# Optimization experiments

Measured on AMD Instinct MI355X. Metric: run time of the kernel, lower is better.

## Reference

```python
import jax, jax.numpy as jnp
import numpy as np
import math

IN_FEATURES = 4096
OUT_FEATURES = 4096
TOKENS = 8192


def hadamard(x):
    """Orthonormal fast Walsh-Hadamard transform along last dim (power of two)."""
    n = x.shape[-1]
    orig_shape = x.shape
    y = x.reshape(-1, n)
    h = 1
    while h < n:  # log2(n) butterfly steps (static loop, n known at trace time)
        y = y.reshape(-1, n // (2 * h), 2 * h)
        left = y[..., :h]
        right = y[..., h:2 * h]
        y = jnp.concatenate([left + right, left - right], axis=-1)
        y = y.reshape(-1, n)
        h *= 2
    return (y / math.sqrt(n)).reshape(orig_shape)


def setup_inputs() -> dict:
    key = jax.random.key(0)
    k1, k2, k3, k4 = jax.random.split(key, 4)
    x = jax.random.normal(k1, (TOKENS, IN_FEATURES), dtype=jnp.float32)
    # int8-valued quantized weights, stored as int32 for portability
    Q_tilde = jax.random.randint(k2, (OUT_FEATURES, IN_FEATURES), -127, 128, dtype=jnp.int32)
    # per-row scales, positive, realistic magnitude (~max_abs/127)
    s_tilde = jax.random.uniform(k3, (OUT_FEATURES, 1), dtype=jnp.float32, minval=0.001, maxval=0.02)
    bias = jax.random.normal(k4, (OUT_FEATURES,), dtype=jnp.float32)
    return {"x": x, "Q_tilde": Q_tilde, "s_tilde": s_tilde, "bias": bias}


def reference(x, Q_tilde, s_tilde, bias):
    # y = hadamard(x) @ (Q * s)^T + bias
    xh = hadamard(x)                                      # [T, in]
    W = Q_tilde.astype(jnp.float32) * s_tilde             # [out, in] dequantized
    y = xh @ W.T + bias                                   # [T, out]
    return y
```

## Files before the change

### kernel.cpp

```cpp
#include <hip/hip_runtime.h>
#include <hip/hip_bf16.h>

typedef int   i32x4 __attribute__((ext_vector_type(4)));
typedef unsigned int   u32;
typedef unsigned short u16;
typedef signed char    i8;

#define TOKENS 8192
#define NDIM   4096
#define KDIM   4096
#define BK     64
#define NKT    (KDIM / BK)

__global__ __launch_bounds__(64)
void fwht_rows_q8(const float* __restrict__ x, i8* __restrict__ xq,
                  float* __restrict__ xscale) {
  const int row = blockIdx.x;
  const int l   = threadIdx.x;

  const float4* xv = reinterpret_cast<const float4*>(x + (size_t)row * KDIM) + l * 16;
  float v[64];
#pragma unroll
  for (int j = 0; j < 16; ++j) {
    float4 f = xv[j];
    v[4*j+0] = f.x; v[4*j+1] = f.y; v[4*j+2] = f.z; v[4*j+3] = f.w;
  }

#pragma unroll
  for (int h = 1; h < 64; h <<= 1) {
#pragma unroll
    for (int j = 0; j < 64; ++j) {
      if ((j & h) == 0) {
        float a = v[j], b = v[j + h];
        v[j] = a + b; v[j + h] = a - b;
      }
    }
  }

#pragma unroll
  for (int m = 1; m < 64; m <<= 1) {
    const bool up = (l & m) != 0;
#pragma unroll
    for (int j = 0; j < 64; ++j) {
      float p = __shfl_xor(v[j], m, 64);
      v[j] = up ? (p - v[j]) : (v[j] + p);
    }
  }

  float mxu = 0.f;
#pragma unroll
  for (int j = 0; j < 64; ++j) mxu = fmaxf(mxu, fabsf(v[j]));
#pragma unroll
  for (int m = 1; m < 64; m <<= 1) mxu = fmaxf(mxu, __shfl_xor(mxu, m, 64));
  mxu = fmaxf(mxu, 1e-30f);
  const float inv = 127.0f / mxu;

  i8* orow = xq + (size_t)row * KDIM + l * 64;
#pragma unroll
  for (int g = 0; g < 4; ++g) {
    u32 w[4];
#pragma unroll
    for (int q4 = 0; q4 < 4; ++q4) {
      int b0 = __float2int_rn(v[g*16+q4*4+0] * inv);
      int b1 = __float2int_rn(v[g*16+q4*4+1] * inv);
      int b2 = __float2int_rn(v[g*16+q4*4+2] * inv);
      int b3 = __float2int_rn(v[g*16+q4*4+3] * inv);
      b0 = min(127, max(-127, b0)); b1 = min(127, max(-127, b1));
      b2 = min(127, max(-127, b2)); b3 = min(127, max(-127, b3));
      w[q4] = (u32)(b0 & 0xff) | ((u32)(b1 & 0xff) << 8) |
              ((u32)(b2 & 0xff) << 16) | ((u32)(b3 & 0xff) << 24);
    }
    uint4 pk; pk.x = w[0]; pk.y = w[1]; pk.z = w[2]; pk.w = w[3];
    *reinterpret_cast<uint4*>(orow + g * 16) = pk;
  }
  if (l == 0) xscale[row] = mxu * (0.015625f / 127.0f);
}

__device__ __forceinline__ u32 pack4(int4 q) {
  return (u32)(q.x & 0xff) | ((u32)(q.y & 0xff) << 8) |
         ((u32)(q.z & 0xff) << 16) | ((u32)(q.w & 0xff) << 24);
}
__global__ __launch_bounds__(256)
void qpack(const int* __restrict__ Q, i8* __restrict__ W8) {
  const size_t idx = ((size_t)blockIdx.x * 256 + threadIdx.x) * 16;
  int4 a = *reinterpret_cast<const int4*>(Q + idx);
  int4 b = *reinterpret_cast<const int4*>(Q + idx + 4);
  int4 c = *reinterpret_cast<const int4*>(Q + idx + 8);
  int4 d = *reinterpret_cast<const int4*>(Q + idx + 12);
  uint4 pk; pk.x = pack4(a); pk.y = pack4(b); pk.z = pack4(c); pk.w = pack4(d);
  *reinterpret_cast<uint4*>(W8 + idx) = pk;
}

__global__ __launch_bounds__(512, 2)
void gemm256_i8(const i8* __restrict__ A, const i8* __restrict__ B,
                const float* __restrict__ xscale, const float* __restrict__ s,
                const float* __restrict__ bias, float* __restrict__ C) {
  __shared__ __align__(16) i8 lds[4 * 32768];

  const int th   = threadIdx.x;
  const int wave = th >> 6;
  const int lane = th & 63;

  const int b0 = blockIdx.x;
  const int xc = b0 & 7;
  const int i  = b0 >> 3;
  const int mt = i >> 1;
  const int nt = xc * 2 + (i & 1);

  const int srow = th >> 2;
  const int scol = ((th & 3) * 16) ^ (((th >> 5) & 1) << 5);
  const i8* gA0 = A + (size_t)(mt * 256 + srow) * KDIM + scol;
  const i8* gA1 = gA0 + (size_t)128 * KDIM;
  const i8* gB0 = B + (size_t)(nt * 256 + srow) * KDIM + scol;
  const i8* gB1 = gB0 + (size_t)128 * KDIM;

  const int ldsA0 = wave * 1024;
  const int ldsA1 = 8192 + wave * 1024;
  const int ldsB0 = 16384 + wave * 1024;
  const int ldsB1 = 24576 + wave * 1024;

#define STAGE_A(tt, ss) do {                                                    \
    __builtin_amdgcn_global_load_lds(                                           \
      (const __attribute__((address_space(1))) void*)(gA0 + (size_t)(tt) * BK), \
      (__attribute__((address_space(3))) void*)(lds + (ss) * 32768 + ldsA0), 16, 0, 0); \
    __builtin_amdgcn_global_load_lds(                                           \
      (const __attribute__((address_space(1))) void*)(gA1 + (size_t)(tt) * BK), \
      (__attribute__((address_space(3))) void*)(lds + (ss) * 32768 + ldsA1), 16, 0, 0); \
  } while (0)
#define STAGE_B(tt, ss) do {                                                    \
    __builtin_amdgcn_global_load_lds(                                           \
      (const __attribute__((address_space(1))) void*)(gB0 + (size_t)(tt) * BK), \
      (__attribute__((address_space(3))) void*)(lds + (ss) * 32768 + ldsB0), 16, 0, 0); \
    __builtin_amdgcn_global_load_lds(                                           \
      (const __attribute__((address_space(1))) void*)(gB1 + (size_t)(tt) * BK), \
      (__attribute__((address_space(3))) void*)(lds + (ss) * 32768 + ldsB1), 16, 0, 0); \
  } while (0)

  const int wm = wave >> 2;
  const int wn = wave & 3;
  const int laneRow = lane & 15;
  const int kByte   = (lane >> 4) << 4;
  const int swz     = ((lane >> 3) & 1) << 5;
  const int aOff = (((wm * 128 + laneRow) * 64 + kByte) ^ swz);
  const int bOff = (((wn * 64 + laneRow) * 64 + kByte) ^ swz) + 16384;

  i32x4 acc[8][4];
#pragma unroll
  for (int mi = 0; mi < 8; ++mi)
#pragma unroll
    for (int ni = 0; ni < 4; ++ni)
      acc[mi][ni] = i32x4{0, 0, 0, 0};

  STAGE_A(0, 0); STAGE_B(0, 0);
  STAGE_A(1, 1); STAGE_B(1, 1);
  asm volatile("s_waitcnt vmcnt(4)" ::: "memory");
  __builtin_amdgcn_sched_barrier(0);
  __builtin_amdgcn_s_barrier();

  for (int t = 0; t < NKT; ++t) {
    const char* base = (const char*)lds + (t & 3) * 32768;
    i32x4 bfr[4], af[4];

#pragma unroll
    for (int ni = 0; ni < 4; ++ni)
      bfr[ni] = *(const i32x4*)(base + bOff + ni * 1024);
#pragma unroll
    for (int mi = 0; mi < 4; ++mi)
      af[mi] = *(const i32x4*)(base + aOff + mi * 1024);
    if (t + 2 < NKT) { STAGE_A(t + 2, (t + 2) & 3); STAGE_B(t + 2, (t + 2) & 3); }
    __builtin_amdgcn_s_barrier();
    asm volatile("s_waitcnt lgkmcnt(0)" ::: "memory");
    __builtin_amdgcn_sched_barrier(0);
    __builtin_amdgcn_s_setprio(1);
#pragma unroll
    for (int mi = 0; mi < 4; ++mi)
#pragma unroll
      for (int ni = 0; ni < 4; ++ni)
        acc[mi][ni] = __builtin_amdgcn_mfma_i32_16x16x64_i8(af[mi], bfr[ni], acc[mi][ni], 0, 0, 0);
    __builtin_amdgcn_s_setprio(0);
    __builtin_amdgcn_s_barrier();

#pragma unroll
    for (int mi = 0; mi < 4; ++mi)
      af[mi] = *(const i32x4*)(base + aOff + 4096 + mi * 1024);
    if (t + 2 < NKT) asm volatile("s_waitcnt vmcnt(4)" ::: "memory");
    else             asm volatile("s_waitcnt vmcnt(0)" ::: "memory");
    __builtin_amdgcn_sched_barrier(0);
    __builtin_amdgcn_s_barrier();
    asm volatile("s_waitcnt lgkmcnt(0)" ::: "memory");
    __builtin_amdgcn_sched_barrier(0);
    __builtin_amdgcn_s_setprio(1);
#pragma unroll
    for (int mi = 0; mi < 4; ++mi)
#pragma unroll
      for (int ni = 0; ni < 4; ++ni)
        acc[mi + 4][ni] = __builtin_amdgcn_mfma_i32_16x16x64_i8(af[mi], bfr[ni], acc[mi + 4][ni], 0, 0, 0);
    __builtin_amdgcn_s_setprio(0);
    __builtin_amdgcn_s_barrier();
  }
#undef STAGE_A
#undef STAGE_B

  const int col0 = nt * 256 + wn * 64 + (lane & 15);
  const int row0 = mt * 256 + wm * 128 + ((lane >> 4) << 2);
  float xs[4][8];
#pragma unroll
  for (int mi = 0; mi < 8; ++mi)
#pragma unroll
    for (int r = 0; r < 4; ++r)
      xs[r][mi] = xscale[row0 + mi * 16 + r];
#pragma unroll
  for (int ni = 0; ni < 4; ++ni) {
    const float sc = s[col0 + ni * 16];
    const float bv = bias[col0 + ni * 16];
#pragma unroll
    for (int mi = 0; mi < 8; ++mi) {
      float* cp = C + (size_t)(row0 + mi * 16) * NDIM + col0 + ni * 16;
#pragma unroll
      for (int r = 0; r < 4; ++r)
        cp[(size_t)r * NDIM] = (float)acc[mi][ni][r] * (xs[r][mi] * sc) + bv;
    }
  }
}

extern "C" void kernel_launch(void* const* d_in, const int* in_sizes, int n_in,
                              void* d_out, int out_size, void* d_ws, size_t ws_size,
                              hipStream_t stream) {
  (void)in_sizes; (void)n_in; (void)out_size; (void)ws_size;
  const float* x    = (const float*)d_in[0];
  const int*   Q    = (const int*)d_in[1];
  const float* s    = (const float*)d_in[2];
  const float* bias = (const float*)d_in[3];
  float* out = (float*)d_out;

  i8*    xq     = (i8*)d_ws;
  i8*    W8     = xq + (size_t)TOKENS * KDIM;
  float* xscale = (float*)(W8 + (size_t)NDIM * KDIM);

  fwht_rows_q8<<<dim3(TOKENS), dim3(64), 0, stream>>>(x, xq, xscale);
  qpack<<<dim3((NDIM * KDIM) / (256 * 16)), dim3(256), 0, stream>>>(Q, W8);
  gemm256_i8<<<dim3((TOKENS / 256) * (NDIM / 256)), dim3(512), 0, stream>>>(
      xq, W8, xscale, s, bias, out);
}
```

Measured before the change: 210.7 us.

## Fuse FWHT and weight-pack kernels; restructure GEMM to BK=128 double-buffered pipeline

Merges the row Hadamard/quantize kernel and the int32-to-int8 weight pack kernel into one launch, using block-index ranges and four rows per 256-thread block. The GEMM now stages 128-wide K tiles into two 64 KB LDS buffers. It software-pipelines the fragment reads by preloading the next tile's A/B registers and interleaving partial lgkmcnt waits with MFMA groups, so each iteration needs one barrier instead of four. The aim is to cut launch overhead and sync stalls. The cost is a shallower two-stage prefetch and more live registers.

```diff
diff --git a/kernel.cpp b/kernel.cpp
--- a/kernel.cpp
+++ b/kernel.cpp
@@ -9,14 +9,29 @@
 #define TOKENS 8192
 #define NDIM   4096
 #define KDIM   4096
-#define BK     64
-#define NKT    (KDIM / BK)
-
-__global__ __launch_bounds__(64)
-void fwht_rows_q8(const float* __restrict__ x, i8* __restrict__ xq,
-                  float* __restrict__ xscale) {
-  const int row = blockIdx.x;
-  const int l   = threadIdx.x;
+#define NKT2   32
+
+__device__ __forceinline__ u32 pack4(int4 q) {
+  return (u32)(q.x & 0xff) | ((u32)(q.y & 0xff) << 8) |
+         ((u32)(q.z & 0xff) << 16) | ((u32)(q.w & 0xff) << 24);
+}
+
+__global__ __launch_bounds__(256)
+void fused_aux(const float* __restrict__ x, i8* __restrict__ xq,
+               float* __restrict__ xscale,
+               const int* __restrict__ Q, i8* __restrict__ W8) {
+  if (blockIdx.x >= 2048) {
+    const size_t idx = (((size_t)(blockIdx.x - 2048)) * 256 + threadIdx.x) * 16;
+    int4 a = *reinterpret_cast<const int4*>(Q + idx);
+    int4 b = *reinterpret_cast<const int4*>(Q + idx + 4);
+    int4 c = *reinterpret_cast<const int4*>(Q + idx + 8);
+    int4 d = *reinterpret_cast<const int4*>(Q + idx + 12);
+    uint4 pk; pk.x = pack4(a); pk.y = pack4(b); pk.z = pack4(c); pk.w = pack4(d);
+    *reinterpret_cast<uint4*>(W8 + idx) = pk;
+    return;
+  }
+  const int row = blockIdx.x * 4 + (threadIdx.x >> 6);
+  const int l   = threadIdx.x & 63;
 
   const float4* xv = reinterpret_cast<const float4*>(x + (size_t)row * KDIM) + l * 16;
   float v[64];
@@ -76,26 +91,11 @@
   if (l == 0) xscale[row] = mxu * (0.015625f / 127.0f);
 }
 
-__device__ __forceinline__ u32 pack4(int4 q) {
-  return (u32)(q.x & 0xff) | ((u32)(q.y & 0xff) << 8) |
-         ((u32)(q.z & 0xff) << 16) | ((u32)(q.w & 0xff) << 24);
-}
-__global__ __launch_bounds__(256)
-void qpack(const int* __restrict__ Q, i8* __restrict__ W8) {
-  const size_t idx = ((size_t)blockIdx.x * 256 + threadIdx.x) * 16;
-  int4 a = *reinterpret_cast<const int4*>(Q + idx);
-  int4 b = *reinterpret_cast<const int4*>(Q + idx + 4);
-  int4 c = *reinterpret_cast<const int4*>(Q + idx + 8);
-  int4 d = *reinterpret_cast<const int4*>(Q + idx + 12);
-  uint4 pk; pk.x = pack4(a); pk.y = pack4(b); pk.z = pack4(c); pk.w = pack4(d);
-  *reinterpret_cast<uint4*>(W8 + idx) = pk;
-}
-
 __global__ __launch_bounds__(512, 2)
-void gemm256_i8(const i8* __restrict__ A, const i8* __restrict__ B,
+void gemm_bk128(const i8* __restrict__ A, const i8* __restrict__ B,
                 const float* __restrict__ xscale, const float* __restrict__ s,
                 const float* __restrict__ bias, float* __restrict__ C) {
-  __shared__ __align__(16) i8 lds[4 * 32768];
+  __shared__ __align__(16) i8 lds[2 * 65536];
 
   const int th   = threadIdx.x;
   const int wave = th >> 6;
@@ -119,21 +119,24 @@
   const int ldsB0 = 16384 + wave * 1024;
   const int ldsB1 = 24576 + wave * 1024;
 
-#define STAGE_A(tt, ss) do {                                                    \
-    __builtin_amdgcn_global_load_lds(                                           \
-      (const __attribute__((address_space(1))) void*)(gA0 + (size_t)(tt) * BK), \
-      (__attribute__((address_space(3))) void*)(lds + (ss) * 32768 + ldsA0), 16, 0, 0); \
-    __builtin_amdgcn_global_load_lds(                                           \
-      (const __attribute__((address_space(1))) void*)(gA1 + (size_t)(tt) * BK), \
-      (__attribute__((address_space(3))) void*)(lds + (ss) * 32768 + ldsA1), 16, 0, 0); \
-  } while (0)
-#define STAGE_B(tt, ss) do {                                                    \
-    __builtin_amdgcn_global_load_lds(                                           \
-      (const __attribute__((address_space(1))) void*)(gB0 + (size_t)(tt) * BK), \
-      (__attribute__((address_space(3))) void*)(lds + (ss) * 32768 + ldsB0), 16, 0, 0); \
-    __builtin_amdgcn_global_load_lds(                                           \
-      (const __attribute__((address_space(1))) void*)(gB1 + (size_t)(tt) * BK), \
-      (__attribute__((address_space(3))) void*)(lds + (ss) * 32768 + ldsB1), 16, 0, 0); \
+#define STAGE(tt, ss) do {                                                       \
+    _Pragma("unroll")                                                             \
+    for (int kk = 0; kk < 2; ++kk) {                                              \
+      const size_t go = (size_t)(tt) * 128 + kk * 64;                             \
+      i8* ldsbase = lds + (ss) * 65536 + kk * 32768;                              \
+      __builtin_amdgcn_global_load_lds(                                           \
+        (const __attribute__((address_space(1))) void*)(gA0 + go),                \
+        (__attribute__((address_space(3))) void*)(ldsbase + ldsA0), 16, 0, 0);    \
+      __builtin_amdgcn_global_load_lds(                                           \
+        (const __attribute__((address_space(1))) void*)(gA1 + go),                \
+        (__attribute__((address_space(3))) void*)(ldsbase + ldsA1), 16, 0, 0);    \
+      __builtin_amdgcn_global_load_lds(                                           \
+        (const __attribute__((address_space(1))) void*)(gB0 + go),                \
+        (__attribute__((address_space(3))) void*)(ldsbase + ldsB0), 16, 0, 0);    \
+      __builtin_amdgcn_global_load_lds(                                           \
+        (const __attribute__((address_space(1))) void*)(gB1 + go),                \
+        (__attribute__((address_space(3))) void*)(ldsbase + ldsB1), 16, 0, 0);    \
+    }                                                                             \
   } while (0)
 
   const int wm = wave >> 2;
@@ -151,55 +154,88 @@
     for (int ni = 0; ni < 4; ++ni)
       acc[mi][ni] = i32x4{0, 0, 0, 0};
 
-  STAGE_A(0, 0); STAGE_B(0, 0);
-  STAGE_A(1, 1); STAGE_B(1, 1);
-  asm volatile("s_waitcnt vmcnt(4)" ::: "memory");
+  i32x4 Ax[4], Ay[4], Bx[4], By[4];
+
+  STAGE(0, 0);
+  STAGE(1, 1);
+  asm volatile("s_waitcnt vmcnt(8)" ::: "memory");
   __builtin_amdgcn_sched_barrier(0);
   __builtin_amdgcn_s_barrier();
-
-  for (int t = 0; t < NKT; ++t) {
-    const char* base = (const char*)lds + (t & 3) * 32768;
-    i32x4 bfr[4], af[4];
-
+  {
+    const char* k0 = (const char*)lds;
+#pragma unroll
+    for (int ni = 0; ni < 4; ++ni) Bx[ni] = *(const i32x4*)(k0 + bOff + ni * 1024);
+#pragma unroll
+    for (int mi = 0; mi < 4; ++mi) Ax[mi] = *(const i32x4*)(k0 + aOff + mi * 1024);
+  }
+
+  for (int t = 0; t < NKT2; ++t) {
+    const char* k0 = (const char*)lds + (t & 1) * 65536;
+    const char* k1 = k0 + 32768;
+    const char* ns = (const char*)lds + ((t + 1) & 1) * 65536;
+
+#pragma unroll
+    for (int mi = 0; mi < 4; ++mi)
+      Ay[mi] = *(const i32x4*)(k0 + aOff + 4096 + mi * 1024);
+    asm volatile("s_waitcnt lgkmcnt(4)" ::: "memory");
+    __builtin_amdgcn_sched_barrier(0);
+    __builtin_amdgcn_s_setprio(1);
+#pragma unroll
+    for (int mi = 0; mi < 4; ++mi)
+#pragma unroll
+      for (int ni = 0; ni < 4; ++ni)
+        acc[mi][ni] = __builtin_amdgcn_mfma_i32_16x16x64_i8(Ax[mi], Bx[ni], acc[mi][ni], 0, 0, 0);
+    __builtin_amdgcn_s_setprio(0);
+
+#pragma unroll
+    for (int mi = 0; mi < 4; ++mi)
+      Ax[mi] = *(const i32x4*)(k1 + aOff + mi * 1024);
 #pragma unroll
     for (int ni = 0; ni < 4; ++ni)
-      bfr[ni] = *(const i32x4*)(base + bOff + ni * 1024);
-#pragma unroll
-    for (int mi = 0; mi < 4; ++mi)
-      af[mi] = *(const i32x4*)(base + aOff + mi * 1024);
-    if (t + 2 < NKT) { STAGE_A(t + 2, (t + 2) & 3); STAGE_B(t + 2, (t + 2) & 3); }
+      By[ni] = *(const i32x4*)(k1 + bOff + ni * 1024);
+    asm volatile("s_waitcnt lgkmcnt(8)" ::: "memory");
+    __builtin_amdgcn_sched_barrier(0);
+    __builtin_amdgcn_s_setprio(1);
+#pragma unroll
+    for (int mi = 0; mi < 4; ++mi)
+#pragma unroll
+      for (int ni = 0; ni < 4; ++ni)
+        acc[mi + 4][ni] = __builtin_amdgcn_mfma_i32_16x16x64_i8(Ay[mi], Bx[ni], acc[mi + 4][ni], 0, 0, 0);
+    __builtin_amdgcn_s_setprio(0);
+
+#pragma unroll
+    for (int mi = 0; mi < 4; ++mi)
+      Ay[mi] = *(const i32x4*)(k1 + aOff + 4096 + mi * 1024);
+    asm volatile("s_waitcnt lgkmcnt(4)" ::: "memory");
+    __builtin_amdgcn_sched_barrier(0);
+    __builtin_amdgcn_s_setprio(1);
+#pragma unroll
+    for (int mi = 0; mi < 4; ++mi)
+#pragma unroll
+      for (int ni = 0; ni < 4; ++ni)
+        acc[mi][ni] = __builtin_amdgcn_mfma_i32_16x16x64_i8(Ax[mi], By[ni], acc[mi][ni], 0, 0, 0);
+    __builtin_amdgcn_s_setprio(0);
+
+    asm volatile("s_waitcnt vmcnt(0)" ::: "memory");
+    asm volatile("s_waitcnt lgkmcnt(0)" ::: "memory");
+    __builtin_amdgcn_sched_barrier(0);
     __builtin_amdgcn_s_barrier();
-    asm volatile("s_waitcnt lgkmcnt(0)" ::: "memory");
-    __builtin_amdgcn_sched_barrier(0);
-    __builtin_amdgcn_s_setprio(1);
-#pragma unroll
-    for (int mi = 0; mi < 4; ++mi)
-#pragma unroll
-      for (int ni = 0; ni < 4; ++ni)
-        acc[mi][ni] = __builtin_amdgcn_mfma_i32_16x16x64_i8(af[mi], bfr[ni], acc[mi][ni], 0, 0, 0);
-    __builtin_amdgcn_s_setprio(0);
-    __builtin_amdgcn_s_barrier();
-
-#pragma unroll
-    for (int mi = 0; mi < 4; ++mi)
-      af[mi] = *(const i32x4*)(base + aOff + 4096 + mi * 1024);
-    if (t + 2 < NKT) asm volatile("s_waitcnt vmcnt(4)" ::: "memory");
-    else             asm volatile("s_waitcnt vmcnt(0)" ::: "memory");
-    __builtin_amdgcn_sched_barrier(0);
-    __builtin_amdgcn_s_barrier();
-    asm volatile("s_waitcnt lgkmcnt(0)" ::: "memory");
-    __builtin_amdgcn_sched_barrier(0);
-    __builtin_amdgcn_s_setprio(1);
-#pragma unroll
-    for (int mi = 0; mi < 4; ++mi)
-#pragma unroll
-      for (int ni = 0; ni < 4; ++ni)
-        acc[mi + 4][ni] = __builtin_amdgcn_mfma_i32_16x16x64_i8(af[mi], bfr[ni], acc[mi + 4][ni], 0, 0, 0);
-    __builtin_amdgcn_s_setprio(0);
-    __builtin_amdgcn_s_barrier();
-  }
-#undef STAGE_A
-#undef STAGE_B
+    if (t + 2 < NKT2) STAGE(t + 2, t & 1);
+    if (t + 1 < NKT2) {
+#pragma unroll
+      for (int ni = 0; ni < 4; ++ni) Bx[ni] = *(const i32x4*)(ns + bOff + ni * 1024);
+#pragma unroll
+      for (int mi = 0; mi < 4; ++mi) Ax[mi] = *(const i32x4*)(ns + aOff + mi * 1024);
+    }
+    __builtin_amdgcn_s_setprio(1);
+#pragma unroll
+    for (int mi = 0; mi < 4; ++mi)
+#pragma unroll
+      for (int ni = 0; ni < 4; ++ni)
+        acc[mi + 4][ni] = __builtin_amdgcn_mfma_i32_16x16x64_i8(Ay[mi], By[ni], acc[mi + 4][ni], 0, 0, 0);
+    __builtin_amdgcn_s_setprio(0);
+  }
+#undef STAGE
 
   const int col0 = nt * 256 + wn * 64 + (lane & 15);
   const int row0 = mt * 256 + wm * 128 + ((lane >> 4) << 2);
@@ -237,8 +273,7 @@
   i8*    W8     = xq + (size_t)TOKENS * KDIM;
   float* xscale = (float*)(W8 + (size_t)NDIM * KDIM);
 
-  fwht_rows_q8<<<dim3(TOKENS), dim3(64), 0, stream>>>(x, xq, xscale);
-  qpack<<<dim3((NDIM * KDIM) / (256 * 16)), dim3(256), 0, stream>>>(Q, W8);
-  gemm256_i8<<<dim3((TOKENS / 256) * (NDIM / 256)), dim3(512), 0, stream>>>(
+  fused_aux<<<dim3(6144), dim3(256), 0, stream>>>(x, xq, xscale, Q, W8);
+  gemm_bk128<<<dim3((TOKENS / 256) * (NDIM / 256)), dim3(512), 0, stream>>>(
       xq, W8, xscale, s, bias, out);
 }
```

Result: faster. 197.2 us (-6.4%).
